# Kernel tuning notes

Measured on AMD Instinct MI355X. Metric: run time of the kernel, lower is better.

The kernel has to match this reference:

```python
import math
import jax, jax.numpy as jnp
import numpy as np

D_MODEL = 1024
NUM_HEADS = 16
NUM_LAYERS = 3
B, S = 2, 1024


def setup_inputs() -> dict:
    key = jax.random.key(0)
    ks = jax.random.split(key, 12)
    std = 1.0 / math.sqrt(2.0 * D_MODEL)  # complex kaiming: per-component std
    wo_std = std / math.sqrt(2.0 * NUM_LAYERS)
    inp = {
        "x_re": jax.random.normal(ks[0], (B, S, D_MODEL), jnp.float32),
        "x_im": jax.random.normal(ks[1], (B, S, D_MODEL), jnp.float32),
        "wq_re": jax.random.normal(ks[2], (D_MODEL, D_MODEL), jnp.float32) * std,
        "wq_im": jax.random.normal(ks[3], (D_MODEL, D_MODEL), jnp.float32) * std,
        "wk_re": jax.random.normal(ks[4], (D_MODEL, D_MODEL), jnp.float32) * std,
        "wk_im": jax.random.normal(ks[5], (D_MODEL, D_MODEL), jnp.float32) * std,
        "wv_re": jax.random.normal(ks[6], (D_MODEL, D_MODEL), jnp.float32) * std,
        "wv_im": jax.random.normal(ks[7], (D_MODEL, D_MODEL), jnp.float32) * std,
        "wo_re": jax.random.normal(ks[8], (D_MODEL, D_MODEL), jnp.float32) * wo_std,
        "wo_im": jax.random.normal(ks[9], (D_MODEL, D_MODEL), jnp.float32) * wo_std,
    }
    return inp


def _forward(x, wq, wk, wv, wo):
    Bx, Sx, D = x.shape
    H = NUM_HEADS
    Dh = D // H

    def proj(w):
        # F.linear(x, w) = x @ w.T ; split heads -> [B,H,S,Dh]
        return (x @ w.T).reshape(Bx, Sx, H, Dh).transpose(0, 2, 1, 3)

    # complex RoPE rotors: e^{i * pos * omega_k}, omega_k = base^{-k/Dh}
    inv_freq = 1.0 / (10000.0 ** (jnp.arange(Dh, dtype=jnp.float32) / Dh))
    angles = jnp.arange(Sx, dtype=jnp.float32)[:, None] * inv_freq[None, :]  # [S,Dh]
    rotors = jax.lax.complex(jnp.cos(angles), jnp.sin(angles))  # [S,Dh]

    Q = proj(wq) * rotors  # broadcast [B,H,S,Dh]
    K = proj(wk) * rotors
    V = proj(wv)

    scale = 1.0 / math.sqrt(Dh)
    # S = Q K^H / sqrt(Dh)  (complex)
    scores = jnp.einsum("bhsd,bhtd->bhst", Q, jnp.conj(K)) * scale
    probs = jax.nn.softmax(scores.real, axis=-1)  # real softmax
    phase = jax.lax.complex(jnp.cos(scores.imag), jnp.sin(scores.imag))  # unit rotors
    attn_weights = probs * phase  # complex [B,H,S,S]

    attn_out = jnp.einsum("bhst,bhtd->bhsd", attn_weights, V)
    attn_out = attn_out.transpose(0, 2, 1, 3).reshape(Bx, Sx, D)
    out = attn_out @ wo.T
    return jnp.stack([out.real, out.imag], axis=-1)  # [B,S,D,2]


def reference(x_re, x_im, wq_re, wq_im, wk_re, wk_im, wv_re, wv_im, wo_re, wo_im):
    x = jax.lax.complex(x_re, x_im)
    wq = jax.lax.complex(wq_re, wq_im)
    wk = jax.lax.complex(wk_re, wk_im)
    wv = jax.lax.complex(wv_re, wv_im)
    wo = jax.lax.complex(wo_re, wo_im)
    return _forward(x, wq, wk, wv, wo)
```

## Files before the change

kernel.cpp:

```cpp
#include <hip/hip_runtime.h>
#include <math.h>

#define S_LEN  1024
#define DMODEL 1024
#define DH     64

typedef float  f4     __attribute__((ext_vector_type(4)));
typedef float  f32x4  __attribute__((ext_vector_type(4)));
typedef __bf16 bf16x2 __attribute__((ext_vector_type(2)));
typedef __bf16 bf16x4 __attribute__((ext_vector_type(4)));
typedef __bf16 bf16x8 __attribute__((ext_vector_type(8)));
typedef unsigned int u32x4 __attribute__((ext_vector_type(4)));

__device__ __forceinline__ bf16x8 neg8(bf16x8 v) {
    u32x4 u;
    __builtin_memcpy(&u, &v, 16);
    u ^= 0x80008000u;
    bf16x8 r;
    __builtin_memcpy(&r, &u, 16);
    return r;
}

__device__ __forceinline__ void gload16(const __bf16* g, __bf16* l) {
    __builtin_amdgcn_global_load_lds(
        (const __attribute__((address_space(1))) void*)g,
        (__attribute__((address_space(3))) void*)l,
        16, 0, 0);
}

__global__ __launch_bounds__(256)
void split_all(const float* __restrict__ xre, const float* __restrict__ xim,
               const float* __restrict__ wqre, const float* __restrict__ wqim,
               const float* __restrict__ wkre, const float* __restrict__ wkim,
               const float* __restrict__ wvre, const float* __restrict__ wvim,
               const float* __restrict__ wore, const float* __restrict__ woim,
               __bf16* __restrict__ xs, __bf16* __restrict__ wqkvs,
               __bf16* __restrict__ wos)
{
    const size_t P1M = (size_t)1024 * 1024;
    const size_t P2M = 2 * P1M;
    const size_t P3M = 3 * P1M;
    const int bid = blockIdx.x;
    const float* re; const float* im; __bf16* dst; size_t plane; int idx;
    if (bid < 1024)      { re = xre;  im = xim;  dst = xs;            plane = P2M; idx = bid*256; }
    else if (bid < 1536) { re = wqre; im = wqim; dst = wqkvs;         plane = P3M; idx = (bid-1024)*256; }
    else if (bid < 2048) { re = wkre; im = wkim; dst = wqkvs + P1M;   plane = P3M; idx = (bid-1536)*256; }
    else if (bid < 2560) { re = wvre; im = wvim; dst = wqkvs + 2*P1M; plane = P3M; idx = (bid-2048)*256; }
    else                 { re = wore; im = woim; dst = wos;           plane = P1M; idx = (bid-2560)*256; }
    idx += threadIdx.x;

    f4 r0 = ((const f4*)re)[idx*2];
    f4 r1 = ((const f4*)re)[idx*2+1];
    f4 i0 = ((const f4*)im)[idx*2];
    f4 i1 = ((const f4*)im)[idx*2+1];
    float rr[8] = {r0.x,r0.y,r0.z,r0.w,r1.x,r1.y,r1.z,r1.w};
    float ii[8] = {i0.x,i0.y,i0.z,i0.w,i1.x,i1.y,i1.z,i1.w};
    bf16x8 hr, lr, hi, li;
    #pragma unroll
    for (int j = 0; j < 8; ++j) {
        __bf16 h = (__bf16)rr[j];
        hr[j] = h; lr[j] = (__bf16)(rr[j] - (float)h);
        __bf16 g = (__bf16)ii[j];
        hi[j] = g; li[j] = (__bf16)(ii[j] - (float)g);
    }
    ((bf16x8*)(dst + 0*plane))[idx] = hr;
    ((bf16x8*)(dst + 1*plane))[idx] = lr;
    ((bf16x8*)(dst + 2*plane))[idx] = hi;
    ((bf16x8*)(dst + 3*plane))[idx] = li;
}

__global__ __launch_bounds__(256, 2)
void cgemm_qkv(const __bf16* __restrict__ A, const __bf16* __restrict__ B,
               __bf16* __restrict__ qp, __bf16* __restrict__ kp,
               __bf16* __restrict__ vt)
{
    __shared__ __bf16 As[2*128*32];
    __shared__ __bf16 Bs[4*64*32];

    const int tid  = threadIdx.x;
    const int lane = tid & 63;
    const int wid  = tid >> 6;
    const int wm   = wid >> 1, wn = wid & 1;
    const int lrow = lane & 15, lk = lane >> 4;
    const int nlin  = blockIdx.x + (blockIdx.y << 4);
    const int xcd   = nlin & 7;
    const int local = nlin >> 3;
    const int m0    = (xcd*2 + (local & 1)) * 128;
    const int n0    = (local >> 1) * 64;
    const int seg   = n0 >> 10;
    const size_t aPlane = (size_t)2048 * 1024;
    const size_t bPlane = (size_t)3072 * 1024;
    const size_t P2M    = (size_t)2048 * 1024;

    const int laneOff = (lane >> 2) * 1024 + (((lane & 3) ^ ((lane >> 3) & 3)) << 3);

    f32x4 accRe[4][2], accIm[4][2];
    #pragma unroll
    for (int i = 0; i < 4; ++i)
        #pragma unroll
        for (int j = 0; j < 2; ++j) {
            accRe[i][j] = (f32x4){0.f,0.f,0.f,0.f};
            accIm[i][j] = (f32x4){0.f,0.f,0.f,0.f};
        }

    const int phys = (lk ^ ((lrow >> 1) & 3)) << 3;

    for (int it = 0; it < 32; ++it) {
        const int k0 = it * 32;
        __syncthreads();
        if (wid < 2) {
            const __bf16* ga = A + (size_t)(wid*2)*aPlane + (size_t)m0*1024 + k0 + laneOff;
            __bf16* la = &As[(wid*128)*32];
            #pragma unroll
            for (int g2 = 0; g2 < 8; ++g2)
                gload16(ga + (size_t)(g2*16)*1024, la + (g2*16)*32);
        } else {
            const __bf16* gb = B + (size_t)((wid-2)*2)*bPlane + (size_t)n0*1024 + k0 + laneOff;
            __bf16* lb = &Bs[((wid-2)*2*64)*32];
            #pragma unroll
            for (int g2 = 0; g2 < 4; ++g2)
                gload16(gb + (size_t)(g2*16)*1024, lb + (g2*16)*32);
            #pragma unroll
            for (int g2 = 0; g2 < 4; ++g2)
                gload16(gb + bPlane + (size_t)(g2*16)*1024, lb + 64*32 + (g2*16)*32);
        }
        __syncthreads();

        bf16x8 bw[2][4];
        #pragma unroll
        for (int nf = 0; nf < 2; ++nf)
            #pragma unroll
            for (int mat = 0; mat < 4; ++mat)
                bw[nf][mat] = *(const bf16x8*)&Bs[(mat*64 + wn*32 + nf*16 + lrow)*32 + phys];
        #pragma unroll
        for (int mf = 0; mf < 4; ++mf) {
            const int arow = wm*64 + mf*16 + lrow;
            bf16x8 xhr = *(const bf16x8*)&As[(0*128 + arow)*32 + phys];
            bf16x8 xhi = *(const bf16x8*)&As[(1*128 + arow)*32 + phys];
            bf16x8 nhi = neg8(xhi);
            if (seg == 2) {
                #pragma unroll
                for (int nf = 0; nf < 2; ++nf) {
                    f32x4 r  = accRe[mf][nf];
                    f32x4 m2 = accIm[mf][nf];
                    r  = __builtin_amdgcn_mfma_f32_16x16x32_bf16(xhr, bw[nf][0], r, 0,0,0);
                    r  = __builtin_amdgcn_mfma_f32_16x16x32_bf16(nhi, bw[nf][2], r, 0,0,0);
                    m2 = __builtin_amdgcn_mfma_f32_16x16x32_bf16(xhr, bw[nf][2], m2, 0,0,0);
                    m2 = __builtin_amdgcn_mfma_f32_16x16x32_bf16(xhi, bw[nf][0], m2, 0,0,0);
                    accRe[mf][nf] = r; accIm[mf][nf] = m2;
                }
            } else {
                #pragma unroll
                for (int nf = 0; nf < 2; ++nf) {
                    f32x4 r  = accRe[mf][nf];
                    f32x4 m2 = accIm[mf][nf];
                    r  = __builtin_amdgcn_mfma_f32_16x16x32_bf16(xhr, bw[nf][0], r, 0,0,0);
                    r  = __builtin_amdgcn_mfma_f32_16x16x32_bf16(xhr, bw[nf][1], r, 0,0,0);
                    r  = __builtin_amdgcn_mfma_f32_16x16x32_bf16(nhi, bw[nf][2], r, 0,0,0);
                    r  = __builtin_amdgcn_mfma_f32_16x16x32_bf16(nhi, bw[nf][3], r, 0,0,0);
                    m2 = __builtin_amdgcn_mfma_f32_16x16x32_bf16(xhr, bw[nf][2], m2, 0,0,0);
                    m2 = __builtin_amdgcn_mfma_f32_16x16x32_bf16(xhr, bw[nf][3], m2, 0,0,0);
                    m2 = __builtin_amdgcn_mfma_f32_16x16x32_bf16(xhi, bw[nf][0], m2, 0,0,0);
                    m2 = __builtin_amdgcn_mfma_f32_16x16x32_bf16(xhi, bw[nf][1], m2, 0,0,0);
                    accRe[mf][nf] = r; accIm[mf][nf] = m2;
                }
            }
        }
    }

    const int nloc = n0 & 1023;
    #pragma unroll
    for (int mf = 0; mf < 4; ++mf) {
        #pragma unroll
        for (int nf = 0; nf < 2; ++nf) {
            const int colB = wn*32 + nf*16 + lrow;
            f32x4 r  = accRe[mf][nf];
            f32x4 m2 = accIm[mf][nf];
            if (seg == 2) {
                const int sBase = m0 + wm*64 + mf*16 + lk*4;
                const int b     = m0 >> 10;
                const int h     = nloc >> 6;
                const int sloc  = sBase & 1023;
                bf16x4 vr, vi;
                #pragma unroll
                for (int rg = 0; rg < 4; ++rg) { vr[rg] = (__bf16)r[rg]; vi[rg] = (__bf16)m2[rg]; }
                size_t off = (size_t)((b*16 + h)*64 + colB) * 1024 + sloc;
                *(bf16x4*)(vt + off)       = vr;
                *(bf16x4*)(vt + P2M + off) = vi;
                continue;
            }
            const float invf = __expf(-(float)colB * 0.14391157f);
            #pragma unroll
            for (int rg = 0; rg < 4; ++rg) {
                const int m = m0 + wm*64 + mf*16 + lk*4 + rg;
                float re = r[rg], im = m2[rg];
                if (seg == 0) { re *= 0.125f; im *= 0.125f; }
                float sn, cs;
                __sincosf((float)(m & (S_LEN-1)) * invf, &sn, &cs);
                float t = re*cs - im*sn;
                im = re*sn + im*cs; re = t;
                __bf16* dp = (seg == 0) ? qp : kp;
                size_t off = (size_t)m*1024 + nloc + colB;
                dp[off]       = (__bf16)re;
                dp[P2M + off] = (__bf16)im;
            }
        }
    }
}

__global__ __launch_bounds__(256, 2)
void cgemm_o(const __bf16* __restrict__ A, const __bf16* __restrict__ B,
             float* __restrict__ outI)
{
    __shared__ __bf16 As[2*128*32];
    __shared__ __bf16 Bs[4*64*32];

    const int tid  = threadIdx.x;
    const int lane = tid & 63;
    const int wid  = tid >> 6;
    const int wm   = wid >> 1, wn = wid & 1;
    const int lrow = lane & 15, lk = lane >> 4;
    const int nlin  = blockIdx.x + (blockIdx.y << 4);
    const int xcd   = nlin & 7;
    const int local = nlin >> 3;
    const int m0    = (xcd*2 + (local & 1)) * 128;
    const int n0    = (local >> 1) * 64;
    const size_t aPlane = (size_t)2048 * 1024;
    const size_t bPlane = (size_t)1024 * 1024;

    f32x4 accRe[4][2], accIm[4][2];
    #pragma unroll
    for (int i = 0; i < 4; ++i)
        #pragma unroll
        for (int j = 0; j < 2; ++j) {
            accRe[i][j] = (f32x4){0.f,0.f,0.f,0.f};
            accIm[i][j] = (f32x4){0.f,0.f,0.f,0.f};
        }

    f4 prA[4], prB[4];
    #pragma unroll
    for (int i = 0; i < 4; ++i) {
        int c = tid + 256*i;
        int mat = c >> 9, row = (c >> 2) & 127, ks = c & 3;
        prA[i] = *(const f4*)(A + (size_t)mat*aPlane + (size_t)(m0+row)*1024 + ks*8);
    }
    #pragma unroll
    for (int i = 0; i < 4; ++i) {
        int c = tid + 256*i;
        int mat = c >> 8, row = (c >> 2) & 63, ks = c & 3;
        prB[i] = *(const f4*)(B + (size_t)mat*bPlane + (size_t)(n0+row)*1024 + ks*8);
    }

    const int phys = (lk ^ ((lrow >> 1) & 3)) << 3;

    for (int it = 0; it < 32; ++it) {
        __syncthreads();
        #pragma unroll
        for (int i = 0; i < 4; ++i) {
            int c = tid + 256*i;
            int mat = c >> 9, row = (c >> 2) & 127, ks = c & 3;
            int wp = (ks ^ ((row >> 1) & 3)) << 3;
            *(f4*)&As[(mat*128 + row)*32 + wp] = prA[i];
        }
        #pragma unroll
        for (int i = 0; i < 4; ++i) {
            int c = tid + 256*i;
            int mat = c >> 8, row = (c >> 2) & 63, ks = c & 3;
            int wp = (ks ^ ((row >> 1) & 3)) << 3;
            *(f4*)&Bs[(mat*64 + row)*32 + wp] = prB[i];
        }
        __syncthreads();
        if (it < 31) {
            const int k0 = (it + 1) * 32;
            #pragma unroll
            for (int i = 0; i < 4; ++i) {
                int c = tid + 256*i;
                int mat = c >> 9, row = (c >> 2) & 127, ks = c & 3;
                prA[i] = *(const f4*)(A + (size_t)mat*aPlane + (size_t)(m0+row)*1024 + k0 + ks*8);
            }
            #pragma unroll
            for (int i = 0; i < 4; ++i) {
                int c = tid + 256*i;
                int mat = c >> 8, row = (c >> 2) & 63, ks = c & 3;
                prB[i] = *(const f4*)(B + (size_t)mat*bPlane + (size_t)(n0+row)*1024 + k0 + ks*8);
            }
        }
        bf16x8 bw[2][4];
        #pragma unroll
        for (int nf = 0; nf < 2; ++nf)
            #pragma unroll
            for (int mat = 0; mat < 4; ++mat)
                bw[nf][mat] = *(const bf16x8*)&Bs[(mat*64 + wn*32 + nf*16 + lrow)*32 + phys];
        #pragma unroll
        for (int mf = 0; mf < 4; ++mf) {
            const int arow = wm*64 + mf*16 + lrow;
            bf16x8 xor_ = *(const bf16x8*)&As[(0*128 + arow)*32 + phys];
            bf16x8 xoi  = *(const bf16x8*)&As[(1*128 + arow)*32 + phys];
            bf16x8 noi  = neg8(xoi);
            #pragma unroll
            for (int nf = 0; nf < 2; ++nf) {
                f32x4 r  = accRe[mf][nf];
                f32x4 m2 = accIm[mf][nf];
                r  = __builtin_amdgcn_mfma_f32_16x16x32_bf16(xor_, bw[nf][0], r, 0,0,0);
                r  = __builtin_amdgcn_mfma_f32_16x16x32_bf16(xor_, bw[nf][1], r, 0,0,0);
                r  = __builtin_amdgcn_mfma_f32_16x16x32_bf16(noi,  bw[nf][2], r, 0,0,0);
                r  = __builtin_amdgcn_mfma_f32_16x16x32_bf16(noi,  bw[nf][3], r, 0,0,0);
                m2 = __builtin_amdgcn_mfma_f32_16x16x32_bf16(xor_, bw[nf][2], m2, 0,0,0);
                m2 = __builtin_amdgcn_mfma_f32_16x16x32_bf16(xor_, bw[nf][3], m2, 0,0,0);
                m2 = __builtin_amdgcn_mfma_f32_16x16x32_bf16(xoi,  bw[nf][0], m2, 0,0,0);
                m2 = __builtin_amdgcn_mfma_f32_16x16x32_bf16(xoi,  bw[nf][1], m2, 0,0,0);
                accRe[mf][nf] = r; accIm[mf][nf] = m2;
            }
        }
    }

    #pragma unroll
    for (int mf = 0; mf < 4; ++mf) {
        #pragma unroll
        for (int nf = 0; nf < 2; ++nf) {
            const int colB = wn*32 + nf*16 + lrow;
            f32x4 r  = accRe[mf][nf];
            f32x4 m2 = accIm[mf][nf];
            #pragma unroll
            for (int rg = 0; rg < 4; ++rg) {
                const int m = m0 + wm*64 + mf*16 + lk*4 + rg;
                size_t off = ((size_t)m*1024 + n0 + colB)*2;
                outI[off] = r[rg]; outI[off+1] = m2[rg];
            }
        }
    }
}

__global__ __launch_bounds__(128, 2)
void flash_mfma(const __bf16* __restrict__ Qp, const __bf16* __restrict__ Kp,
                const __bf16* __restrict__ Vt, __bf16* __restrict__ Os)
{
    __shared__ __align__(16) __bf16 Ks[2][32][72];
    __shared__ __align__(16) __bf16 Vs[2][64][40];
    __shared__ __align__(16) __bf16 Pa[2][16][40];
    __shared__ __align__(16) __bf16 Pb[2][16][40];

    const int tid  = threadIdx.x;
    const int lane = tid & 63;
    const int w    = tid >> 6;
    const int lq   = lane & 15;
    const int g    = lane >> 4;
    const int nlin  = blockIdx.x + (blockIdx.y << 5);
    const int xcd   = nlin & 7;
    const int local = nlin >> 3;
    const int bh    = xcd*4 + (local & 3);
    const int q0    = (local >> 2) * 32;
    const int b     = bh >> 4, h = bh & 15;
    const size_t P2M = (size_t)2048 * 1024;

    bf16x8 qf[2][2];
    {
        const size_t qrow = (size_t)(b*1024 + q0 + w*16 + lq) * 1024 + h*64;
        #pragma unroll
        for (int p = 0; p < 2; ++p)
            #pragma unroll
            for (int kc = 0; kc < 2; ++kc)
                qf[p][kc] = *(const bf16x8*)(Qp + (size_t)p*P2M + qrow + kc*32 + g*8);
    }

    f32x4 oRe[4], oIm[4];
    #pragma unroll
    for (int d = 0; d < 4; ++d) { oRe[d] = (f32x4){0,0,0,0}; oIm[d] = (f32x4){0,0,0,0}; }
    float lsum[4] = {0.f, 0.f, 0.f, 0.f};

    bf16x8 pk[4]; bf16x8 pv[4];
    #pragma unroll
    for (int i = 0; i < 4; ++i) {
        int c = tid + 128*i;
        int p = c >> 8, key = (c >> 3) & 31, cc = c & 7;
        pk[i] = *(const bf16x8*)(Kp + (size_t)p*P2M + (size_t)(b*1024 + key)*1024 + h*64 + cc*8);
    }
    #pragma unroll
    for (int i = 0; i < 4; ++i) {
        int c = tid + 128*i;
        int p = c >> 8, d = (c >> 2) & 63, cc = c & 3;
        pv[i] = *(const bf16x8*)(Vt + (size_t)p*P2M + (size_t)(bh*64 + d)*1024 + cc*8);
    }

    for (int it = 0; it < 32; ++it) {
        __syncthreads();
        #pragma unroll
        for (int i = 0; i < 4; ++i) {
            int c = tid + 128*i;
            int p = c >> 8, key = (c >> 3) & 31, cc = c & 7;
            int pr = ((key & 1) << 4) | (key >> 1);
            *(bf16x8*)&Ks[p][pr][cc*8] = pk[i];
        }
        #pragma unroll
        for (int i = 0; i < 4; ++i) {
            int c = tid + 128*i;
            int p = c >> 8, d = (c >> 2) & 63, cc = c & 3;
            *(bf16x8*)&Vs[p][d][cc*8] = pv[i];
        }
        if (it < 31) {
            const int t0 = (it + 1) * 32;
            #pragma unroll
            for (int i = 0; i < 4; ++i) {
                int c = tid + 128*i;
                int p = c >> 8, key = (c >> 3) & 31, cc = c & 7;
                pk[i] = *(const bf16x8*)(Kp + (size_t)p*P2M + (size_t)(b*1024 + t0 + key)*1024 + h*64 + cc*8);
            }
            #pragma unroll
            for (int i = 0; i < 4; ++i) {
                int c = tid + 128*i;
                int p = c >> 8, d = (c >> 2) & 63, cc = c & 3;
                pv[i] = *(const bf16x8*)(Vt + (size_t)p*P2M + (size_t)(bh*64 + d)*1024 + t0 + cc*8);
            }
        }
        __syncthreads();

        f32x4 sRe[2], sIm[2];
        #pragma unroll
        for (int f = 0; f < 2; ++f) { sRe[f] = (f32x4){0,0,0,0}; sIm[f] = (f32x4){0,0,0,0}; }
        __builtin_amdgcn_s_setprio(1);
        #pragma unroll
        for (int kc = 0; kc < 2; ++kc) {
            #pragma unroll
            for (int f = 0; f < 2; ++f) {
                const int key = f*16 + lq;
                bf16x8 kr = *(const bf16x8*)&Ks[0][key][kc*32 + g*8];
                bf16x8 ki = *(const bf16x8*)&Ks[1][key][kc*32 + g*8];
                bf16x8 nki = neg8(ki);
                f32x4 r = sRe[f], m2 = sIm[f];
                r  = __builtin_amdgcn_mfma_f32_16x16x32_bf16(qf[0][kc], kr,  r, 0,0,0);
                r  = __builtin_amdgcn_mfma_f32_16x16x32_bf16(qf[1][kc], ki,  r, 0,0,0);
                m2 = __builtin_amdgcn_mfma_f32_16x16x32_bf16(qf[1][kc], kr,  m2, 0,0,0);
                m2 = __builtin_amdgcn_mfma_f32_16x16x32_bf16(qf[0][kc], nki, m2, 0,0,0);
                sRe[f] = r; sIm[f] = m2;
            }
        }
        __builtin_amdgcn_s_setprio(0);

        #pragma unroll
        for (int i = 0; i < 4; ++i) {
            float p0 = __expf(sRe[0][i] - 8.f);
            float p1 = __expf(sRe[1][i] - 8.f);
            lsum[i] += p0 + p1;
            float sn0, cs0, sn1, cs1;
            __sincosf(sIm[0][i], &sn0, &cs0);
            __sincosf(sIm[1][i], &sn1, &cs1);
            const int row = g*4 + i;
            ((bf16x2*)&Pa[w][row][0])[lq] = (bf16x2){(__bf16)(p0*cs0), (__bf16)(p1*cs1)};
            ((bf16x2*)&Pb[w][row][0])[lq] = (bf16x2){(__bf16)(p0*sn0), (__bf16)(p1*sn1)};
        }

        bf16x8 pa  = *(const bf16x8*)&Pa[w][lq][g*8];
        bf16x8 pb  = *(const bf16x8*)&Pb[w][lq][g*8];
        bf16x8 npb = neg8(pb);
        __builtin_amdgcn_s_setprio(1);
        #pragma unroll
        for (int df = 0; df < 4; ++df) {
            bf16x8 vr = *(const bf16x8*)&Vs[0][df*16 + lq][g*8];
            bf16x8 vi = *(const bf16x8*)&Vs[1][df*16 + lq][g*8];
            oRe[df] = __builtin_amdgcn_mfma_f32_16x16x32_bf16(pa,  vr, oRe[df], 0,0,0);
            oRe[df] = __builtin_amdgcn_mfma_f32_16x16x32_bf16(npb, vi, oRe[df], 0,0,0);
            oIm[df] = __builtin_amdgcn_mfma_f32_16x16x32_bf16(pa,  vi, oIm[df], 0,0,0);
            oIm[df] = __builtin_amdgcn_mfma_f32_16x16x32_bf16(pb,  vr, oIm[df], 0,0,0);
        }
        __builtin_amdgcn_s_setprio(0);
    }

    #pragma unroll
    for (int i = 0; i < 4; ++i) {
        #pragma unroll
        for (int mm = 1; mm < 16; mm <<= 1)
            lsum[i] += __shfl_xor(lsum[i], mm, 16);
    }

    #pragma unroll
    for (int i = 0; i < 4; ++i) {
        const float inv = 1.f / lsum[i];
        const size_t rowOff = (size_t)(b*1024 + q0 + w*16 + g*4 + i) * 1024 + h*64;
        #pragma unroll
        for (int df = 0; df < 4; ++df) {
            size_t off = rowOff + df*16 + lq;
            Os[off]       = (__bf16)(oRe[df][i] * inv);
            Os[P2M + off] = (__bf16)(oIm[df][i] * inv);
        }
    }
}

extern "C" void kernel_launch(void* const* d_in, const int* in_sizes, int n_in,
                              void* d_out, int out_size, void* d_ws, size_t ws_size,
                              hipStream_t stream)
{
    (void)in_sizes; (void)n_in; (void)out_size; (void)ws_size;
    const float* x_re  = (const float*)d_in[0];
    const float* x_im  = (const float*)d_in[1];
    const float* wq_re = (const float*)d_in[2];
    const float* wq_im = (const float*)d_in[3];
    const float* wk_re = (const float*)d_in[4];
    const float* wk_im = (const float*)d_in[5];
    const float* wv_re = (const float*)d_in[6];
    const float* wv_im = (const float*)d_in[7];
    const float* wo_re = (const float*)d_in[8];
    const float* wo_im = (const float*)d_in[9];
    float* out = (float*)d_out;

    char* wsb = (char*)d_ws;
    const size_t MB = (size_t)1 << 20;
    __bf16* x_s    = (__bf16*)(wsb +  0*MB);
    __bf16* Os_g   = (__bf16*)(wsb +  0*MB);
    __bf16* wqkv_s = (__bf16*)(wsb + 16*MB);
    __bf16* wo_s   = (__bf16*)(wsb + 40*MB);
    __bf16* Qs_g   = (__bf16*)(wsb + 48*MB);
    __bf16* Ks_g   = (__bf16*)(wsb + 64*MB);
    __bf16* Vt_g   = (__bf16*)(wsb + 80*MB);

    split_all<<<3072, 256, 0, stream>>>(x_re, x_im, wq_re, wq_im, wk_re, wk_im,
                                        wv_re, wv_im, wo_re, wo_im,
                                        x_s, wqkv_s, wo_s);
    cgemm_qkv<<<dim3(16, 48), 256, 0, stream>>>(x_s, wqkv_s, Qs_g, Ks_g, Vt_g);
    flash_mfma<<<dim3(32, 32), 128, 0, stream>>>(Qs_g, Ks_g, Vt_g, Os_g);
    cgemm_o<<<dim3(16, 16), 256, 0, stream>>>(Os_g, wo_s, out);
}
```

Baseline: 185.1 us.

## Double flash-attention key tile to 64 and drop unused x low-part planes

The attention kernel now processes 64 keys per iteration instead of 32. It enlarges the K/V/P shared-memory tiles and prefetch registers and splits the PV product into two 32-wide chunks, so it runs half as many loop iterations and barriers. The split kernel also stops writing the bf16 residual planes for x, which the projection GEMM never read, and the GEMM's A-plane indexing is updated to match. The larger tiles raise register and LDS pressure, which may reduce occupancy.

```diff
diff --git a/kernel.cpp b/kernel.cpp
--- a/kernel.cpp
+++ b/kernel.cpp
@@ -42,7 +42,8 @@
     const size_t P3M = 3 * P1M;
     const int bid = blockIdx.x;
     const float* re; const float* im; __bf16* dst; size_t plane; int idx;
-    if (bid < 1024)      { re = xre;  im = xim;  dst = xs;            plane = P2M; idx = bid*256; }
+    bool xcase = false;
+    if (bid < 1024)      { re = xre;  im = xim;  dst = xs;            plane = P2M; idx = bid*256; xcase = true; }
     else if (bid < 1536) { re = wqre; im = wqim; dst = wqkvs;         plane = P3M; idx = (bid-1024)*256; }
     else if (bid < 2048) { re = wkre; im = wkim; dst = wqkvs + P1M;   plane = P3M; idx = (bid-1536)*256; }
     else if (bid < 2560) { re = wvre; im = wvim; dst = wqkvs + 2*P1M; plane = P3M; idx = (bid-2048)*256; }
@@ -63,10 +64,15 @@
         __bf16 g = (__bf16)ii[j];
         hi[j] = g; li[j] = (__bf16)(ii[j] - (float)g);
     }
-    ((bf16x8*)(dst + 0*plane))[idx] = hr;
-    ((bf16x8*)(dst + 1*plane))[idx] = lr;
-    ((bf16x8*)(dst + 2*plane))[idx] = hi;
-    ((bf16x8*)(dst + 3*plane))[idx] = li;
+    if (xcase) {
+        ((bf16x8*)(dst + 0*plane))[idx] = hr;
+        ((bf16x8*)(dst + 1*plane))[idx] = hi;
+    } else {
+        ((bf16x8*)(dst + 0*plane))[idx] = hr;
+        ((bf16x8*)(dst + 1*plane))[idx] = lr;
+        ((bf16x8*)(dst + 2*plane))[idx] = hi;
+        ((bf16x8*)(dst + 3*plane))[idx] = li;
+    }
 }
 
 __global__ __launch_bounds__(256, 2)
@@ -109,7 +115,7 @@
         const int k0 = it * 32;
         __syncthreads();
         if (wid < 2) {
-            const __bf16* ga = A + (size_t)(wid*2)*aPlane + (size_t)m0*1024 + k0 + laneOff;
+            const __bf16* ga = A + (size_t)wid*aPlane + (size_t)m0*1024 + k0 + laneOff;
             __bf16* la = &As[(wid*128)*32];
             #pragma unroll
             for (int g2 = 0; g2 < 8; ++g2)
@@ -335,10 +341,10 @@
 void flash_mfma(const __bf16* __restrict__ Qp, const __bf16* __restrict__ Kp,
                 const __bf16* __restrict__ Vt, __bf16* __restrict__ Os)
 {
-    __shared__ __align__(16) __bf16 Ks[2][32][72];
-    __shared__ __align__(16) __bf16 Vs[2][64][40];
-    __shared__ __align__(16) __bf16 Pa[2][16][40];
-    __shared__ __align__(16) __bf16 Pb[2][16][40];
+    __shared__ __align__(16) __bf16 Ks[2][64][72];
+    __shared__ __align__(16) __bf16 Vs[2][64][72];
+    __shared__ __align__(16) __bf16 Pa[2][16][72];
+    __shared__ __align__(16) __bf16 Pb[2][16][72];
 
     const int tid  = threadIdx.x;
     const int lane = tid & 63;
@@ -368,63 +374,63 @@
     for (int d = 0; d < 4; ++d) { oRe[d] = (f32x4){0,0,0,0}; oIm[d] = (f32x4){0,0,0,0}; }
     float lsum[4] = {0.f, 0.f, 0.f, 0.f};
 
-    bf16x8 pk[4]; bf16x8 pv[4];
-    #pragma unroll
-    for (int i = 0; i < 4; ++i) {
+    bf16x8 pk[8]; bf16x8 pv[8];
+    #pragma unroll
+    for (int i = 0; i < 8; ++i) {
         int c = tid + 128*i;
-        int p = c >> 8, key = (c >> 3) & 31, cc = c & 7;
+        int p = c >> 9, key = (c >> 3) & 63, cc = c & 7;
         pk[i] = *(const bf16x8*)(Kp + (size_t)p*P2M + (size_t)(b*1024 + key)*1024 + h*64 + cc*8);
     }
     #pragma unroll
-    for (int i = 0; i < 4; ++i) {
+    for (int i = 0; i < 8; ++i) {
         int c = tid + 128*i;
-        int p = c >> 8, d = (c >> 2) & 63, cc = c & 3;
+        int p = c >> 9, d = (c >> 3) & 63, cc = c & 7;
         pv[i] = *(const bf16x8*)(Vt + (size_t)p*P2M + (size_t)(bh*64 + d)*1024 + cc*8);
     }
 
-    for (int it = 0; it < 32; ++it) {
+    for (int it = 0; it < 16; ++it) {
         __syncthreads();
         #pragma unroll
-        for (int i = 0; i < 4; ++i) {
+        for (int i = 0; i < 8; ++i) {
             int c = tid + 128*i;
-            int p = c >> 8, key = (c >> 3) & 31, cc = c & 7;
-            int pr = ((key & 1) << 4) | (key >> 1);
+            int p = c >> 9, key = (c >> 3) & 63, cc = c & 7;
+            int pr = ((key & 1) << 5) | (key >> 1);
             *(bf16x8*)&Ks[p][pr][cc*8] = pk[i];
         }
         #pragma unroll
-        for (int i = 0; i < 4; ++i) {
+        for (int i = 0; i < 8; ++i) {
             int c = tid + 128*i;
-            int p = c >> 8, d = (c >> 2) & 63, cc = c & 3;
+            int p = c >> 9, d = (c >> 3) & 63, cc = c & 7;
             *(bf16x8*)&Vs[p][d][cc*8] = pv[i];
         }
-        if (it < 31) {
-            const int t0 = (it + 1) * 32;
-            #pragma unroll
-            for (int i = 0; i < 4; ++i) {
+        if (it < 15) {
+            const int t0 = (it + 1) * 64;
+            #pragma unroll
+            for (int i = 0; i < 8; ++i) {
                 int c = tid + 128*i;
-                int p = c >> 8, key = (c >> 3) & 31, cc = c & 7;
+                int p = c >> 9, key = (c >> 3) & 63, cc = c & 7;
                 pk[i] = *(const bf16x8*)(Kp + (size_t)p*P2M + (size_t)(b*1024 + t0 + key)*1024 + h*64 + cc*8);
             }
             #pragma unroll
-            for (int i = 0; i < 4; ++i) {
+            for (int i = 0; i < 8; ++i) {
                 int c = tid + 128*i;
-                int p = c >> 8, d = (c >> 2) & 63, cc = c & 3;
+                int p = c >> 9, d = (c >> 3) & 63, cc = c & 7;
                 pv[i] = *(const bf16x8*)(Vt + (size_t)p*P2M + (size_t)(bh*64 + d)*1024 + t0 + cc*8);
             }
         }
         __syncthreads();
 
-        f32x4 sRe[2], sIm[2];
-        #pragma unroll
-        for (int f = 0; f < 2; ++f) { sRe[f] = (f32x4){0,0,0,0}; sIm[f] = (f32x4){0,0,0,0}; }
+        f32x4 sRe[4], sIm[4];
+        #pragma unroll
+        for (int f = 0; f < 4; ++f) { sRe[f] = (f32x4){0,0,0,0}; sIm[f] = (f32x4){0,0,0,0}; }
         __builtin_amdgcn_s_setprio(1);
         #pragma unroll
         for (int kc = 0; kc < 2; ++kc) {
             #pragma unroll
-            for (int f = 0; f < 2; ++f) {
-                const int key = f*16 + lq;
-                bf16x8 kr = *(const bf16x8*)&Ks[0][key][kc*32 + g*8];
-                bf16x8 ki = *(const bf16x8*)&Ks[1][key][kc*32 + g*8];
+            for (int f = 0; f < 4; ++f) {
+                const int prow = f*16 + lq;
+                bf16x8 kr = *(const bf16x8*)&Ks[0][prow][kc*32 + g*8];
+                bf16x8 ki = *(const bf16x8*)&Ks[1][prow][kc*32 + g*8];
                 bf16x8 nki = neg8(ki);
                 f32x4 r = sRe[f], m2 = sIm[f];
                 r  = __builtin_amdgcn_mfma_f32_16x16x32_bf16(qf[0][kc], kr,  r, 0,0,0);
@@ -439,28 +445,37 @@
         #pragma unroll
         for (int i = 0; i < 4; ++i) {
             float p0 = __expf(sRe[0][i] - 8.f);
-            float p1 = __expf(sRe[1][i] - 8.f);
-            lsum[i] += p0 + p1;
-            float sn0, cs0, sn1, cs1;
+            float p1 = __expf(sRe[2][i] - 8.f);
+            float p2 = __expf(sRe[1][i] - 8.f);
+            float p3 = __expf(sRe[3][i] - 8.f);
+            lsum[i] += (p0 + p1) + (p2 + p3);
+            float sn0, cs0, sn1, cs1, sn2, cs2, sn3, cs3;
             __sincosf(sIm[0][i], &sn0, &cs0);
-            __sincosf(sIm[1][i], &sn1, &cs1);
+            __sincosf(sIm[2][i], &sn1, &cs1);
+            __sincosf(sIm[1][i], &sn2, &cs2);
+            __sincosf(sIm[3][i], &sn3, &cs3);
             const int row = g*4 + i;
-            ((bf16x2*)&Pa[w][row][0])[lq] = (bf16x2){(__bf16)(p0*cs0), (__bf16)(p1*cs1)};
-            ((bf16x2*)&Pb[w][row][0])[lq] = (bf16x2){(__bf16)(p0*sn0), (__bf16)(p1*sn1)};
-        }
-
-        bf16x8 pa  = *(const bf16x8*)&Pa[w][lq][g*8];
-        bf16x8 pb  = *(const bf16x8*)&Pb[w][lq][g*8];
-        bf16x8 npb = neg8(pb);
+            ((bf16x2*)&Pa[w][row][0])[lq]  = (bf16x2){(__bf16)(p0*cs0), (__bf16)(p1*cs1)};
+            ((bf16x2*)&Pb[w][row][0])[lq]  = (bf16x2){(__bf16)(p0*sn0), (__bf16)(p1*sn1)};
+            ((bf16x2*)&Pa[w][row][32])[lq] = (bf16x2){(__bf16)(p2*cs2), (__bf16)(p3*cs3)};
+            ((bf16x2*)&Pb[w][row][32])[lq] = (bf16x2){(__bf16)(p2*sn2), (__bf16)(p3*sn3)};
+        }
+
         __builtin_amdgcn_s_setprio(1);
         #pragma unroll
-        for (int df = 0; df < 4; ++df) {
-            bf16x8 vr = *(const bf16x8*)&Vs[0][df*16 + lq][g*8];
-            bf16x8 vi = *(const bf16x8*)&Vs[1][df*16 + lq][g*8];
-            oRe[df] = __builtin_amdgcn_mfma_f32_16x16x32_bf16(pa,  vr, oRe[df], 0,0,0);
-            oRe[df] = __builtin_amdgcn_mfma_f32_16x16x32_bf16(npb, vi, oRe[df], 0,0,0);
-            oIm[df] = __builtin_amdgcn_mfma_f32_16x16x32_bf16(pa,  vi, oIm[df], 0,0,0);
-            oIm[df] = __builtin_amdgcn_mfma_f32_16x16x32_bf16(pb,  vr, oIm[df], 0,0,0);
+        for (int kc2 = 0; kc2 < 2; ++kc2) {
+            bf16x8 pa  = *(const bf16x8*)&Pa[w][lq][kc2*32 + g*8];
+            bf16x8 pb  = *(const bf16x8*)&Pb[w][lq][kc2*32 + g*8];
+            bf16x8 npb = neg8(pb);
+            #pragma unroll
+            for (int df = 0; df < 4; ++df) {
+                bf16x8 vr = *(const bf16x8*)&Vs[0][df*16 + lq][kc2*32 + g*8];
+                bf16x8 vi = *(const bf16x8*)&Vs[1][df*16 + lq][kc2*32 + g*8];
+                oRe[df] = __builtin_amdgcn_mfma_f32_16x16x32_bf16(pa,  vr, oRe[df], 0,0,0);
+                oRe[df] = __builtin_amdgcn_mfma_f32_16x16x32_bf16(npb, vi, oRe[df], 0,0,0);
+                oIm[df] = __builtin_amdgcn_mfma_f32_16x16x32_bf16(pa,  vi, oIm[df], 0,0,0);
+                oIm[df] = __builtin_amdgcn_mfma_f32_16x16x32_bf16(pb,  vr, oIm[df], 0,0,0);
+            }
         }
         __builtin_amdgcn_s_setprio(0);
     }
```

New measurement: 197.9 us. +6.9%, slower.
